# Kernel optimization log

Hardware: AMD Instinct MI355X
Metric: run time of the kernel (lower is better)

## Reference

```python
import jax, jax.numpy as jnp
import numpy as np

NUM_HEADS = 4
LN_EPS = 1e-5
L2_EPS = 1e-12


def setup_inputs() -> dict:
    key = jax.random.key(0)
    ks = jax.random.split(key, 10)
    B, L, D, Hd = 256, 197, 768, 512
    dh = Hd // NUM_HEADS  # 128
    NC = 1000
    sc = lambda k, shape, s: jax.random.normal(k, shape, jnp.float32) * s
    return {
        "cls_token": jax.random.normal(ks[0], (B, D), jnp.float32),
        "x": jax.random.normal(ks[1], (B, L, D), jnp.float32),
        "proj_w": sc(ks[2], (D, Hd), 0.02),
        "proj_b": jnp.zeros((Hd,), jnp.float32),
        "ln_g": jnp.ones((dh,), jnp.float32),
        "ln_b": jnp.zeros((dh,), jnp.float32),
        "conv1_w": sc(ks[3], (3, 3, 3, 3), 0.2),
        "conv2_w": sc(ks[4], (3, 3, 3, 3), 0.2),
        "cls1_w": sc(ks[5], (D, NC), 0.02),
        "cls1_b": jnp.zeros((NC,), jnp.float32),
        "cls2_w": sc(ks[6], (2883, NC), 0.02),
        "cls2_b": jnp.zeros((NC,), jnp.float32),
    }


def reference(cls_token, x, proj_w, proj_b, ln_g, ln_b, conv1_w, conv2_w,
              cls1_w, cls1_b, cls2_w, cls2_b):
    B, L, D = x.shape
    dh = ln_g.shape[0]
    # proj on patch tokens (drop cls at position 0)
    xp = x[:, 1:, :] @ proj_w + proj_b            # (B, 196, 512)
    Lp = xp.shape[1]
    H = xp.shape[2] // dh
    heads = xp.reshape(B, Lp, H, dh).transpose(2, 0, 1, 3)  # (H, B, Lp, dh)
    # LayerNorm over last dim (eps=1e-5, biased var, affine)
    mu = heads.mean(-1, keepdims=True)
    var = heads.var(-1, keepdims=True)
    hn = (heads - mu) * jax.lax.rsqrt(var + LN_EPS) * ln_g + ln_b
    # Covariance._remove_mean: adaptive_avg_pool2d on (B, dh, Lp) -> mean over BOTH dh and Lp per sample
    hn = hn - hn.mean(axis=(2, 3), keepdims=True)
    # 'near' cross-covariances between adjacent heads, all pairs batched
    x1, x2 = hn[:-1], hn[1:]                      # (H-1, B, Lp, dh)
    cov = jnp.einsum('pbnd,pbne->pbde', x1, x2) / Lp  # (H-1, B, dh, dh)
    # L2 normalize over dim=2 (row axis of each dh x dh map), F.normalize eps
    nrm = jnp.sqrt(jnp.sum(cov * cov, axis=2, keepdims=True))
    cov = cov / jnp.maximum(nrm, L2_EPS)
    cov = cov.transpose(1, 0, 2, 3)               # (B, 3, 128, 128)
    conv = lambda z, w: jax.lax.conv_general_dilated(
        z, w, (2, 2), 'VALID', dimension_numbers=('NCHW', 'OIHW', 'NCHW'))
    z = conv(cov, conv1_w)                        # (B, 3, 63, 63)
    z = jax.nn.gelu(z, approximate=False)
    z = conv(z, conv2_w)                          # (B, 3, 31, 31)
    flat = z.reshape(B, -1)                       # (B, 2883)
    out = ((cls_token @ cls1_w + cls1_b) + (flat @ cls2_w + cls2_b)) / 2
    return out
```

## Files before the change

kernel.cpp:

```cpp
#include <hip/hip_runtime.h>
#include <hip/hip_bf16.h>
#include <cstdint>

typedef __bf16 bf16_t;
typedef __bf16 bf16x4 __attribute__((ext_vector_type(4)));
typedef __bf16 bf16x8 __attribute__((ext_vector_type(8)));
typedef float floatx4 __attribute__((ext_vector_type(4)));

#define LNEPS 1e-5f

__device__ inline void async_copy16(const bf16_t* g, bf16_t* l) {
    __builtin_amdgcn_global_load_lds((const __attribute__((address_space(1))) void*)g,
                                     (__attribute__((address_space(3))) void*)l,
                                     16, 0, 0);
}

__global__ __launch_bounds__(256)
void k_cvt_x(const float* __restrict__ x, bf16_t* __restrict__ xbf, int b0) {
    const int vid = blockIdx.x * 256 + threadIdx.x;
    const int row = vid / 192;
    const int kv  = vid - row * 192;
    const int b = b0 + row / 196, l = row - (row / 196) * 196;
    const floatx4 f = *(const floatx4*)(x + ((b * 197 + l + 1) * 192 + kv) * 4);
    bf16x4 o;
#pragma unroll
    for (int e = 0; e < 4; e++) o[e] = (bf16_t)f[e];
    *(bf16x4*)(xbf + vid * 4) = o;
}

__global__ __launch_bounds__(256)
void k_transpose_w(const float* __restrict__ w, bf16_t* __restrict__ wt) {
    __shared__ bf16_t tile[32][33];
    const int bx = blockIdx.x;
    const int by = blockIdx.y;
    const int tx = threadIdx.x & 31, ty = threadIdx.x >> 5;
    for (int i = ty; i < 32; i += 8)
        tile[i][tx] = (bf16_t)w[(by*32 + i)*512 + bx*32 + tx];
    __syncthreads();
    for (int i = ty; i < 32; i += 8)
        wt[(bx*32 + i)*768 + by*32 + tx] = tile[tx][i];
}

__global__ __launch_bounds__(256, 2)
void k_proj_ln(const bf16_t* __restrict__ xbf, const bf16_t* __restrict__ wt,
               const float* __restrict__ pb, const float* __restrict__ lng,
               const float* __restrict__ lnb, bf16_t* __restrict__ hn, int m_base)
{
    __shared__ bf16_t As[128*32];
    __shared__ bf16_t Bs[128*32];
    __shared__ float rs_sum[2][128];
    __shared__ float rs_sq[2][128];

    const int t = threadIdx.x;
    const int lane = t & 63;
    const int wv = t >> 6;
    const int wr = wv >> 1, wc = wv & 1;
    const int q = lane >> 4;
    const int c = lane & 15;
    const int h = blockIdx.y;
    const int mt = blockIdx.x;

    const int srow  = t >> 2;
    const int skoff = (t & 3) * 8;
    const int m0 = mt * 128;
    const bf16_t* ag0 = xbf + (m0 + srow) * 768 + skoff;
    const bf16_t* ag1 = xbf + (m0 + srow + 64) * 768 + skoff;
    const bf16_t* bg0 = wt + (h*128 + srow)*768 + skoff;
    const bf16_t* bg1 = wt + (h*128 + srow + 64)*768 + skoff;

    floatx4 acc[4][4];
#pragma unroll
    for (int i = 0; i < 4; i++)
#pragma unroll
        for (int j = 0; j < 4; j++)
#pragma unroll
            for (int r = 0; r < 4; r++) acc[i][j][r] = 0.f;

    for (int k0 = 0; k0 < 768; k0 += 32) {
        __syncthreads();
        async_copy16(ag0 + k0, &As[t*8]);
        async_copy16(ag1 + k0, &As[2048 + t*8]);
        async_copy16(bg0 + k0, &Bs[t*8]);
        async_copy16(bg1 + k0, &Bs[2048 + t*8]);
        __syncthreads();
        bf16x8 af[4], bfr[4];
#pragma unroll
        for (int i = 0; i < 4; i++)
            af[i] = *(const bf16x8*)&As[(wr*64 + i*16 + c)*32 + q*8];
#pragma unroll
        for (int j = 0; j < 4; j++)
            bfr[j] = *(const bf16x8*)&Bs[(wc*64 + j*16 + c)*32 + q*8];
#pragma unroll
        for (int i = 0; i < 4; i++)
#pragma unroll
            for (int j = 0; j < 4; j++)
                acc[i][j] = __builtin_amdgcn_mfma_f32_16x16x32_bf16(af[i], bfr[j], acc[i][j], 0, 0, 0);
    }

    float bias[4], gg[4], bb[4];
#pragma unroll
    for (int j = 0; j < 4; j++) {
        const int d = wc*64 + j*16 + c;
        bias[j] = pb[h*128 + d];
        gg[j]   = lng[d];
        bb[j]   = lnb[d];
    }
#pragma unroll
    for (int i = 0; i < 4; i++)
#pragma unroll
        for (int j = 0; j < 4; j++)
#pragma unroll
            for (int r = 0; r < 4; r++) acc[i][j][r] += bias[j];

#pragma unroll
    for (int i = 0; i < 4; i++) {
#pragma unroll
        for (int r = 0; r < 4; r++) {
            float s = 0.f, s2 = 0.f;
#pragma unroll
            for (int j = 0; j < 4; j++) { const float v = acc[i][j][r]; s += v; s2 += v*v; }
#pragma unroll
            for (int o = 1; o < 16; o <<= 1) { s += __shfl_xor(s, o); s2 += __shfl_xor(s2, o); }
            if (c == 0) {
                const int row = wr*64 + i*16 + q*4 + r;
                rs_sum[wc][row] = s;
                rs_sq[wc][row]  = s2;
            }
        }
    }
    __syncthreads();
#pragma unroll
    for (int i = 0; i < 4; i++) {
#pragma unroll
        for (int r = 0; r < 4; r++) {
            const int row = wr*64 + i*16 + q*4 + r;
            const float mu = (rs_sum[0][row] + rs_sum[1][row]) * (1.f/128.f);
            const float ms = (rs_sq[0][row]  + rs_sq[1][row])  * (1.f/128.f);
            const float rstd = rsqrtf(ms - mu*mu + LNEPS);
            const int gm = m_base + m0 + row;
            const int bI = gm / 196, l = gm - bI*196;
            bf16_t* dst = hn + (((h*256 + bI)*196 + l) << 7);
#pragma unroll
            for (int j = 0; j < 4; j++) {
                const float v = (acc[i][j][r] - mu)*rstd*gg[j] + bb[j];
                dst[wc*64 + j*16 + c] = (bf16_t)v;
            }
        }
    }
}

__global__ __launch_bounds__(256, 2)
void k_cov(const bf16_t* __restrict__ hn, float* __restrict__ cov)
{
    __shared__ bf16_t x1s[128*40];
    __shared__ bf16_t x2s[128*40];
    __shared__ float rs1[128], rs2[128];
    __shared__ float colsq[2][128];
    __shared__ float nrm_inv[128];
    __shared__ float mu_s[2];

    const int t = threadIdx.x;
    const int lane = t & 63;
    const int wv = t >> 6;
    const int wr = wv >> 1, wc = wv & 1;
    const int q = lane >> 4;
    const int c = lane & 15;
    const int b = blockIdx.x;
    const int p = blockIdx.y;

    const bf16_t* X1 = hn + (((p*256 + b)*196) << 7);
    const bf16_t* X2 = hn + ((((p+1)*256 + b)*196) << 7);

    {
        const bf16_t* S = (t < 128) ? X1 : X2;
        const int d = t & 127;
        float s = 0.f;
        for (int n = 0; n < 196; n++) s += (float)S[(n << 7) + d];
        if (t < 128) rs1[d] = s; else rs2[d] = s;
    }
    __syncthreads();
    if (wv == 0) {
        float s = rs1[lane] + rs1[lane + 64];
#pragma unroll
        for (int o = 1; o < 64; o <<= 1) s += __shfl_xor(s, o);
        if (lane == 0) mu_s[0] = s * (1.f/(196.f*128.f));
    } else if (wv == 1) {
        float s = rs2[lane] + rs2[lane + 64];
#pragma unroll
        for (int o = 1; o < 64; o <<= 1) s += __shfl_xor(s, o);
        if (lane == 0) mu_s[1] = s * (1.f/(196.f*128.f));
    }

    floatx4 acc[4][4];
#pragma unroll
    for (int i = 0; i < 4; i++)
#pragma unroll
        for (int j = 0; j < 4; j++)
#pragma unroll
            for (int r = 0; r < 4; r++) acc[i][j][r] = 0.f;

    const int nl = t >> 3;
    const int d0 = (t & 7) * 16;

    for (int n0 = 0; n0 < 224; n0 += 32) {
        __syncthreads();
        const int n = n0 + nl;
        bf16x8 va, vb, wa, wb;
        if (n < 196) {
            const bf16_t* s1 = X1 + (n << 7) + d0;
            const bf16_t* s2 = X2 + (n << 7) + d0;
            va = *(const bf16x8*)s1;
            vb = *(const bf16x8*)(s1 + 8);
            wa = *(const bf16x8*)s2;
            wb = *(const bf16x8*)(s2 + 8);
        } else {
#pragma unroll
            for (int e = 0; e < 8; e++) {
                va[e] = (bf16_t)0.f; vb[e] = (bf16_t)0.f;
                wa[e] = (bf16_t)0.f; wb[e] = (bf16_t)0.f;
            }
        }
#pragma unroll
        for (int e = 0; e < 8; e++) {
            x1s[(d0 + e)*40 + nl]     = va[e];
            x1s[(d0 + 8 + e)*40 + nl] = vb[e];
            x2s[(d0 + e)*40 + nl]     = wa[e];
            x2s[(d0 + 8 + e)*40 + nl] = wb[e];
        }
        __syncthreads();
        bf16x8 af[4], bfr[4];
#pragma unroll
        for (int i = 0; i < 4; i++)
            af[i] = *(const bf16x8*)&x1s[(wr*64 + i*16 + c)*40 + q*8];
#pragma unroll
        for (int j = 0; j < 4; j++)
            bfr[j] = *(const bf16x8*)&x2s[(wc*64 + j*16 + c)*40 + q*8];
#pragma unroll
        for (int i = 0; i < 4; i++)
#pragma unroll
            for (int j = 0; j < 4; j++)
                acc[i][j] = __builtin_amdgcn_mfma_f32_16x16x32_bf16(af[i], bfr[j], acc[i][j], 0, 0, 0);
    }

    const float mu1 = mu_s[0], mu2 = mu_s[1];
    const float invL = 1.f/196.f;
    float csq[4] = {0.f, 0.f, 0.f, 0.f};
#pragma unroll
    for (int i = 0; i < 4; i++)
#pragma unroll
        for (int j = 0; j < 4; j++)
#pragma unroll
            for (int r = 0; r < 4; r++) {
                const int d = wr*64 + i*16 + q*4 + r;
                const int e = wc*64 + j*16 + c;
                const float v = acc[i][j][r]*invL - mu2*rs1[d]*invL - mu1*rs2[e]*invL + mu1*mu2;
                acc[i][j][r] = v;
                csq[j] += v*v;
            }
#pragma unroll
    for (int j = 0; j < 4; j++) {
        float s = csq[j];
        s += __shfl_xor(s, 16);
        s += __shfl_xor(s, 32);
        csq[j] = s;
    }
    if (q == 0) {
#pragma unroll
        for (int j = 0; j < 4; j++) colsq[wr][wc*64 + j*16 + c] = csq[j];
    }
    __syncthreads();
    if (t < 128) {
        const float nr = sqrtf(colsq[0][t] + colsq[1][t]);
        nrm_inv[t] = 1.f / fmaxf(nr, 1e-12f);
    }
    __syncthreads();
    float* dst = cov + ((long)b*3 + p)*16384;
#pragma unroll
    for (int i = 0; i < 4; i++)
#pragma unroll
        for (int j = 0; j < 4; j++) {
            const int e = wc*64 + j*16 + c;
            const float ni = nrm_inv[e];
#pragma unroll
            for (int r = 0; r < 4; r++) {
                const int d = wr*64 + i*16 + q*4 + r;
                dst[(d << 7) + e] = acc[i][j][r] * ni;
            }
        }
}

__global__ __launch_bounds__(256)
void k_conv1(const float* __restrict__ cov, const float* __restrict__ w1,
             float* __restrict__ z1)
{
    __shared__ float W[27];
    const int t = threadIdx.x;
    const int b = blockIdx.x, o = blockIdx.y;
    if (t < 27) W[t] = w1[o*27 + t];
    __syncthreads();
    const float* C = cov + (long)b*3*16384;
    float* Z = z1 + ((long)b*3 + o)*3969;
    for (int idx = t; idx < 3969; idx += 256) {
        const int y = idx / 63, xx = idx - y*63;
        float a = 0.f;
#pragma unroll
        for (int i = 0; i < 3; i++) {
            const float* Ci = C + i*16384 + (2*y)*128 + 2*xx;
            const float* Wi = &W[i*9];
            a += Ci[0]*Wi[0]   + Ci[1]*Wi[1]   + Ci[2]*Wi[2]
               + Ci[128]*Wi[3] + Ci[129]*Wi[4] + Ci[130]*Wi[5]
               + Ci[256]*Wi[6] + Ci[257]*Wi[7] + Ci[258]*Wi[8];
        }
        Z[idx] = 0.5f*a*(1.0f + erff(a*0.70710678118654752f));
    }
}

__global__ __launch_bounds__(256)
void k_conv2(const float* __restrict__ z1, const float* __restrict__ w2,
             bf16_t* __restrict__ Xb)
{
    __shared__ float Z[3*3969];
    __shared__ float W[81];
    const int t = threadIdx.x, b = blockIdx.x;
    if (t < 81) W[t] = w2[t];
    const float* src = z1 + (long)b*3*3969;
    for (int idx = t; idx < 3*3969; idx += 256) Z[idx] = src[idx];
    __syncthreads();
    for (int idx = t; idx < 2883; idx += 256) {
        const int o = idx / 961, rem = idx - o*961;
        const int y = rem / 31, xx = rem - y*31;
        float a = 0.f;
#pragma unroll
        for (int i = 0; i < 3; i++) {
            const float* Zi = Z + i*3969 + (2*y)*63 + 2*xx;
            const float* Wi = &W[(o*3+i)*9];
            a += Zi[0]*Wi[0]   + Zi[1]*Wi[1]   + Zi[2]*Wi[2]
               + Zi[63]*Wi[3]  + Zi[64]*Wi[4]  + Zi[65]*Wi[5]
               + Zi[126]*Wi[6] + Zi[127]*Wi[7] + Zi[128]*Wi[8];
        }
        Xb[(long)b*3712 + 768 + idx] = (bf16_t)a;
    }
}

__global__ __launch_bounds__(256)
void k_cvt_cls(const float* __restrict__ cls, bf16_t* __restrict__ Xb)
{
    const int t = threadIdx.x, b = blockIdx.x;
    for (int k = t; k < 768; k += 256)
        Xb[b*3712 + k] = (bf16_t)cls[b*768 + k];
    if (t < 61) Xb[b*3712 + 3651 + t] = (bf16_t)0.f;
}

__global__ __launch_bounds__(256)
void k_cvt_w(const float* __restrict__ W1, const float* __restrict__ W2,
             bf16_t* __restrict__ Wb)
{
    __shared__ bf16_t tile[32][33];
    const int k0 = blockIdx.x * 32;
    const int n0 = blockIdx.y * 32;
    const int tx = threadIdx.x & 31, ty = threadIdx.x >> 5;
    for (int i = ty; i < 32; i += 8) {
        const int k = k0 + i, n = n0 + tx;
        float v = 0.f;
        if (n < 1000 && k < 3651)
            v = (k < 768) ? W1[k*1000 + n] : W2[(k-768)*1000 + n];
        tile[i][tx] = (bf16_t)v;
    }
    __syncthreads();
    for (int i = ty; i < 32; i += 8)
        Wb[(n0 + i)*3712 + k0 + tx] = tile[tx][i];
}

__global__ __launch_bounds__(256, 2)
void k_gemm_cls(const bf16_t* __restrict__ Xb, const bf16_t* __restrict__ Wb,
                float* __restrict__ partial)
{
    __shared__ bf16_t As[128*32];
    __shared__ bf16_t Bs[128*32];

    const int t = threadIdx.x;
    const int lane = t & 63;
    const int wv = t >> 6;
    const int wr = wv >> 1, wc = wv & 1;
    const int q = lane >> 4;
    const int c = lane & 15;
    const int nt = blockIdx.x;
    const int mt = blockIdx.y;
    const int sp = blockIdx.z;

    const int srow  = t >> 2;
    const int skoff = (t & 3) * 8;
    const int m0 = mt * 128, n0 = nt * 128;
    const int kbase = sp * 928;
    const bf16_t* ag0 = Xb + (m0 + srow) * 3712 + kbase + skoff;
    const bf16_t* ag1 = Xb + (m0 + srow + 64) * 3712 + kbase + skoff;
    const bf16_t* bg0 = Wb + (n0 + srow) * 3712 + kbase + skoff;
    const bf16_t* bg1 = Wb + (n0 + srow + 64) * 3712 + kbase + skoff;

    floatx4 acc[4][4];
#pragma unroll
    for (int i = 0; i < 4; i++)
#pragma unroll
        for (int j = 0; j < 4; j++)
#pragma unroll
            for (int r = 0; r < 4; r++) acc[i][j][r] = 0.f;

    for (int k0 = 0; k0 < 928; k0 += 32) {
        __syncthreads();
        async_copy16(ag0 + k0, &As[t*8]);
        async_copy16(ag1 + k0, &As[2048 + t*8]);
        async_copy16(bg0 + k0, &Bs[t*8]);
        async_copy16(bg1 + k0, &Bs[2048 + t*8]);
        __syncthreads();
        bf16x8 af[4], bfr[4];
#pragma unroll
        for (int i = 0; i < 4; i++)
            af[i] = *(const bf16x8*)&As[(wr*64 + i*16 + c)*32 + q*8];
#pragma unroll
        for (int j = 0; j < 4; j++)
            bfr[j] = *(const bf16x8*)&Bs[(wc*64 + j*16 + c)*32 + q*8];
#pragma unroll
        for (int i = 0; i < 4; i++)
#pragma unroll
            for (int j = 0; j < 4; j++)
                acc[i][j] = __builtin_amdgcn_mfma_f32_16x16x32_bf16(af[i], bfr[j], acc[i][j], 0, 0, 0);
    }

    float* base = partial + ((long)sp*256 + m0)*1024 + n0;
#pragma unroll
    for (int i = 0; i < 4; i++)
#pragma unroll
        for (int r = 0; r < 4; r++) {
            const int row = wr*64 + i*16 + q*4 + r;
#pragma unroll
            for (int j = 0; j < 4; j++)
                base[row*1024 + wc*64 + j*16 + c] = acc[i][j][r];
        }
}

__global__ __launch_bounds__(256)
void k_cls_fin(const float* __restrict__ partial, const float* __restrict__ b1,
               const float* __restrict__ b2, float* __restrict__ out)
{
    const int idx = blockIdx.x * 256 + threadIdx.x;
    const int m = idx / 1000, n = idx - m*1000;
    float s = partial[(m)*1024 + n] + partial[(256 + m)*1024 + n]
            + partial[(512 + m)*1024 + n] + partial[(768 + m)*1024 + n];
    out[idx] = 0.5f*(s + b1[n] + b2[n]);
}

extern "C" void kernel_launch(void* const* d_in, const int* in_sizes, int n_in,
                              void* d_out, int out_size, void* d_ws, size_t ws_size,
                              hipStream_t stream) {
    const float* cls = (const float*)d_in[0];
    const float* x   = (const float*)d_in[1];
    const float* pw  = (const float*)d_in[2];
    const float* pb  = (const float*)d_in[3];
    const float* lng = (const float*)d_in[4];
    const float* lnb = (const float*)d_in[5];
    const float* c1w = (const float*)d_in[6];
    const float* c2w = (const float*)d_in[7];
    const float* w1  = (const float*)d_in[8];
    const float* b1  = (const float*)d_in[9];
    const float* w2  = (const float*)d_in[10];
    const float* b2  = (const float*)d_in[11];

    char* ws = (char*)d_ws;
    bf16_t* hn    = (bf16_t*)(ws);
    bf16_t* xbfh  = (bf16_t*)(ws + 51380224ull);
    bf16_t* wt    = (bf16_t*)(ws + 89915392ull);
    float*  covb  = (float*) (ws + 51380224ull);
    float*  z1    = (float*) (ws);
    bf16_t* Xb    = (bf16_t*)(ws + 101711872ull);
    bf16_t* Wb    = (bf16_t*)(ws + 103612416ull);
    float*  part  = (float*) (ws + 111214592ull);
    float*  out   = (float*)d_out;

    k_transpose_w<<<dim3(16, 24), 256, 0, stream>>>(pw, wt);
    k_cvt_x<<<18816, 256, 0, stream>>>(x, xbfh, 0);
    k_proj_ln<<<dim3(196, 4), 256, 0, stream>>>(xbfh, wt, pb, lng, lnb, hn, 0);
    k_cvt_x<<<18816, 256, 0, stream>>>(x, xbfh, 128);
    k_proj_ln<<<dim3(196, 4), 256, 0, stream>>>(xbfh, wt, pb, lng, lnb, hn, 25088);
    k_cvt_cls<<<256, 256, 0, stream>>>(cls, Xb);
    k_cvt_w<<<dim3(116, 32), 256, 0, stream>>>(w1, w2, Wb);
    k_cov<<<dim3(256, 3), 256, 0, stream>>>(hn, covb);
    k_conv1<<<dim3(256, 3), 256, 0, stream>>>(covb, c1w, z1);
    k_conv2<<<256, 256, 0, stream>>>(z1, c2w, Xb);
    k_gemm_cls<<<dim3(8, 2, 4), 256, 0, stream>>>(Xb, Wb, part);
    k_cls_fin<<<1000, 256, 0, stream>>>(part, b1, b2, out);
}
```

Measured before the change: 441.1 us.

## Widen proj tile to two heads, fuse convs, precompute column sums

The x conversion now runs once over the whole batch with 8-wide vectors instead of two half-batch passes, and the projection GEMM runs as a single launch. Each projection block now covers two full heads (256 columns), so each wave owns one head and can do the LayerNorm reduction with shuffles alone, dropping the shared-memory row-stat pass and its barrier. A separate column-sum kernel precomputes per-sample sums so the covariance kernel no longer does a serial 196-row scan twice per block. conv1 and conv2 are fused so the GELU output stays in shared memory instead of going through global memory. The cost is a doubled accumulator array per thread (more VGPR pressure at 2 blocks/SM) and a larger workspace footprint.

```diff
diff --git a/kernel.cpp b/kernel.cpp
--- a/kernel.cpp
+++ b/kernel.cpp
@@ -16,16 +16,18 @@
 }
 
 __global__ __launch_bounds__(256)
-void k_cvt_x(const float* __restrict__ x, bf16_t* __restrict__ xbf, int b0) {
+void k_cvt_x(const float* __restrict__ x, bf16_t* __restrict__ xbf) {
     const int vid = blockIdx.x * 256 + threadIdx.x;
-    const int row = vid / 192;
-    const int kv  = vid - row * 192;
-    const int b = b0 + row / 196, l = row - (row / 196) * 196;
-    const floatx4 f = *(const floatx4*)(x + ((b * 197 + l + 1) * 192 + kv) * 4);
-    bf16x4 o;
-#pragma unroll
-    for (int e = 0; e < 4; e++) o[e] = (bf16_t)f[e];
-    *(bf16x4*)(xbf + vid * 4) = o;
+    const int row = vid / 96;
+    const int kv  = vid - row * 96;
+    const int b = row / 196, l = row - (row / 196) * 196;
+    const float* src = x + ((b * 197 + l + 1) * 96 + kv) * 8;
+    const floatx4 f0 = *(const floatx4*)src;
+    const floatx4 f1 = *(const floatx4*)(src + 4);
+    bf16x8 o;
+#pragma unroll
+    for (int e = 0; e < 4; e++) { o[e] = (bf16_t)f0[e]; o[e+4] = (bf16_t)f1[e]; }
+    *(bf16x8*)(xbf + vid * 8) = o;
 }
 
 __global__ __launch_bounds__(256)
@@ -44,12 +46,10 @@
 __global__ __launch_bounds__(256, 2)
 void k_proj_ln(const bf16_t* __restrict__ xbf, const bf16_t* __restrict__ wt,
                const float* __restrict__ pb, const float* __restrict__ lng,
-               const float* __restrict__ lnb, bf16_t* __restrict__ hn, int m_base)
+               const float* __restrict__ lnb, bf16_t* __restrict__ hn)
 {
     __shared__ bf16_t As[128*32];
-    __shared__ bf16_t Bs[128*32];
-    __shared__ float rs_sum[2][128];
-    __shared__ float rs_sq[2][128];
+    __shared__ bf16_t Bs[256*32];
 
     const int t = threadIdx.x;
     const int lane = t & 63;
@@ -57,22 +57,20 @@
     const int wr = wv >> 1, wc = wv & 1;
     const int q = lane >> 4;
     const int c = lane & 15;
-    const int h = blockIdx.y;
-    const int mt = blockIdx.x;
+    const int hp = blockIdx.y;
+    const int m0 = blockIdx.x * 128;
 
     const int srow  = t >> 2;
     const int skoff = (t & 3) * 8;
-    const int m0 = mt * 128;
     const bf16_t* ag0 = xbf + (m0 + srow) * 768 + skoff;
-    const bf16_t* ag1 = xbf + (m0 + srow + 64) * 768 + skoff;
-    const bf16_t* bg0 = wt + (h*128 + srow)*768 + skoff;
-    const bf16_t* bg1 = wt + (h*128 + srow + 64)*768 + skoff;
-
-    floatx4 acc[4][4];
-#pragma unroll
-    for (int i = 0; i < 4; i++)
-#pragma unroll
-        for (int j = 0; j < 4; j++)
+    const bf16_t* ag1 = ag0 + 64*768;
+    const bf16_t* bg0 = wt + (hp*256 + srow)*768 + skoff;
+
+    floatx4 acc[4][8];
+#pragma unroll
+    for (int i = 0; i < 4; i++)
+#pragma unroll
+        for (int j = 0; j < 8; j++)
 #pragma unroll
             for (int r = 0; r < 4; r++) acc[i][j][r] = 0.f;
 
@@ -80,77 +78,80 @@
         __syncthreads();
         async_copy16(ag0 + k0, &As[t*8]);
         async_copy16(ag1 + k0, &As[2048 + t*8]);
-        async_copy16(bg0 + k0, &Bs[t*8]);
-        async_copy16(bg1 + k0, &Bs[2048 + t*8]);
-        __syncthreads();
-        bf16x8 af[4], bfr[4];
+        async_copy16(bg0 + k0,            &Bs[t*8]);
+        async_copy16(bg0 + 64*768 + k0,   &Bs[2048 + t*8]);
+        async_copy16(bg0 + 128*768 + k0,  &Bs[4096 + t*8]);
+        async_copy16(bg0 + 192*768 + k0,  &Bs[6144 + t*8]);
+        __syncthreads();
+        bf16x8 af[4], bfr[8];
 #pragma unroll
         for (int i = 0; i < 4; i++)
             af[i] = *(const bf16x8*)&As[(wr*64 + i*16 + c)*32 + q*8];
 #pragma unroll
-        for (int j = 0; j < 4; j++)
-            bfr[j] = *(const bf16x8*)&Bs[(wc*64 + j*16 + c)*32 + q*8];
-#pragma unroll
-        for (int i = 0; i < 4; i++)
-#pragma unroll
-            for (int j = 0; j < 4; j++)
+        for (int j = 0; j < 8; j++)
+            bfr[j] = *(const bf16x8*)&Bs[(wc*128 + j*16 + c)*32 + q*8];
+#pragma unroll
+        for (int i = 0; i < 4; i++)
+#pragma unroll
+            for (int j = 0; j < 8; j++)
                 acc[i][j] = __builtin_amdgcn_mfma_f32_16x16x32_bf16(af[i], bfr[j], acc[i][j], 0, 0, 0);
     }
 
-    float bias[4], gg[4], bb[4];
-#pragma unroll
-    for (int j = 0; j < 4; j++) {
-        const int d = wc*64 + j*16 + c;
+    const int h = hp*2 + wc;
+    float bias[8], gg[8], bb[8];
+#pragma unroll
+    for (int j = 0; j < 8; j++) {
+        const int d = j*16 + c;
         bias[j] = pb[h*128 + d];
         gg[j]   = lng[d];
         bb[j]   = lnb[d];
     }
 #pragma unroll
-    for (int i = 0; i < 4; i++)
-#pragma unroll
-        for (int j = 0; j < 4; j++)
-#pragma unroll
-            for (int r = 0; r < 4; r++) acc[i][j][r] += bias[j];
-
-#pragma unroll
     for (int i = 0; i < 4; i++) {
 #pragma unroll
         for (int r = 0; r < 4; r++) {
             float s = 0.f, s2 = 0.f;
 #pragma unroll
-            for (int j = 0; j < 4; j++) { const float v = acc[i][j][r]; s += v; s2 += v*v; }
+            for (int j = 0; j < 8; j++) {
+                const float v = acc[i][j][r] + bias[j];
+                acc[i][j][r] = v;
+                s += v; s2 += v*v;
+            }
 #pragma unroll
             for (int o = 1; o < 16; o <<= 1) { s += __shfl_xor(s, o); s2 += __shfl_xor(s2, o); }
-            if (c == 0) {
-                const int row = wr*64 + i*16 + q*4 + r;
-                rs_sum[wc][row] = s;
-                rs_sq[wc][row]  = s2;
-            }
-        }
-    }
-    __syncthreads();
-#pragma unroll
-    for (int i = 0; i < 4; i++) {
-#pragma unroll
-        for (int r = 0; r < 4; r++) {
-            const int row = wr*64 + i*16 + q*4 + r;
-            const float mu = (rs_sum[0][row] + rs_sum[1][row]) * (1.f/128.f);
-            const float ms = (rs_sq[0][row]  + rs_sq[1][row])  * (1.f/128.f);
+            const float mu = s * (1.f/128.f);
+            const float ms = s2 * (1.f/128.f);
             const float rstd = rsqrtf(ms - mu*mu + LNEPS);
-            const int gm = m_base + m0 + row;
+            const int gm = m0 + wr*64 + i*16 + q*4 + r;
             const int bI = gm / 196, l = gm - bI*196;
             bf16_t* dst = hn + (((h*256 + bI)*196 + l) << 7);
 #pragma unroll
-            for (int j = 0; j < 4; j++) {
+            for (int j = 0; j < 8; j++) {
                 const float v = (acc[i][j][r] - mu)*rstd*gg[j] + bb[j];
-                dst[wc*64 + j*16 + c] = (bf16_t)v;
+                dst[j*16 + c] = (bf16_t)v;
             }
         }
     }
 }
 
+__global__ __launch_bounds__(256)
+void k_colsum(const bf16_t* __restrict__ hn, float* __restrict__ colsum)
+{
+    __shared__ float tmp[2][128];
+    const int t = threadIdx.x;
+    const int d = t & 127, half = t >> 7;
+    const bf16_t* S = hn + ((long)blockIdx.x * 196 << 7);
+    float s = 0.f;
+    const int n0 = half * 98;
+    for (int n = 0; n < 98; n++) s += (float)S[((n0 + n) << 7) + d];
+    tmp[half][d] = s;
+    __syncthreads();
+    if (t < 128) colsum[(blockIdx.x << 7) + t] = tmp[0][t] + tmp[1][t];
+}
+
 __global__ __launch_bounds__(256, 2)
-void k_cov(const bf16_t* __restrict__ hn, float* __restrict__ cov)
+void k_cov(const bf16_t* __restrict__ hn, const float* __restrict__ colsum,
+           float* __restrict__ cov)
 {
     __shared__ bf16_t x1s[128*40];
     __shared__ bf16_t x2s[128*40];
@@ -171,13 +172,8 @@
     const bf16_t* X1 = hn + (((p*256 + b)*196) << 7);
     const bf16_t* X2 = hn + ((((p+1)*256 + b)*196) << 7);
 
-    {
-        const bf16_t* S = (t < 128) ? X1 : X2;
-        const int d = t & 127;
-        float s = 0.f;
-        for (int n = 0; n < 196; n++) s += (float)S[(n << 7) + d];
-        if (t < 128) rs1[d] = s; else rs2[d] = s;
-    }
+    if (t < 128) rs1[t] = colsum[((p*256 + b) << 7) + t];
+    else         rs2[t & 127] = colsum[(((p+1)*256 + b) << 7) + (t & 127)];
     __syncthreads();
     if (wv == 0) {
         float s = rs1[lane] + rs1[lane + 64];
@@ -290,41 +286,30 @@
 }
 
 __global__ __launch_bounds__(256)
-void k_conv1(const float* __restrict__ cov, const float* __restrict__ w1,
-             float* __restrict__ z1)
-{
-    __shared__ float W[27];
-    const int t = threadIdx.x;
-    const int b = blockIdx.x, o = blockIdx.y;
-    if (t < 27) W[t] = w1[o*27 + t];
+void k_convs(const float* __restrict__ cov, const float* __restrict__ w1,
+             const float* __restrict__ w2, bf16_t* __restrict__ Xb)
+{
+    __shared__ float Z[3*3969];
+    __shared__ float W1s[81];
+    __shared__ float W2s[81];
+    const int t = threadIdx.x, b = blockIdx.x;
+    if (t < 81) { W1s[t] = w1[t]; W2s[t] = w2[t]; }
     __syncthreads();
     const float* C = cov + (long)b*3*16384;
-    float* Z = z1 + ((long)b*3 + o)*3969;
-    for (int idx = t; idx < 3969; idx += 256) {
-        const int y = idx / 63, xx = idx - y*63;
+    for (int idx = t; idx < 3*3969; idx += 256) {
+        const int o = idx / 3969, rem = idx - o*3969;
+        const int y = rem / 63, xx = rem - y*63;
         float a = 0.f;
 #pragma unroll
         for (int i = 0; i < 3; i++) {
             const float* Ci = C + i*16384 + (2*y)*128 + 2*xx;
-            const float* Wi = &W[i*9];
+            const float* Wi = &W1s[o*27 + i*9];
             a += Ci[0]*Wi[0]   + Ci[1]*Wi[1]   + Ci[2]*Wi[2]
                + Ci[128]*Wi[3] + Ci[129]*Wi[4] + Ci[130]*Wi[5]
                + Ci[256]*Wi[6] + Ci[257]*Wi[7] + Ci[258]*Wi[8];
         }
         Z[idx] = 0.5f*a*(1.0f + erff(a*0.70710678118654752f));
     }
-}
-
-__global__ __launch_bounds__(256)
-void k_conv2(const float* __restrict__ z1, const float* __restrict__ w2,
-             bf16_t* __restrict__ Xb)
-{
-    __shared__ float Z[3*3969];
-    __shared__ float W[81];
-    const int t = threadIdx.x, b = blockIdx.x;
-    if (t < 81) W[t] = w2[t];
-    const float* src = z1 + (long)b*3*3969;
-    for (int idx = t; idx < 3*3969; idx += 256) Z[idx] = src[idx];
     __syncthreads();
     for (int idx = t; idx < 2883; idx += 256) {
         const int o = idx / 961, rem = idx - o*961;
@@ -333,7 +318,7 @@
 #pragma unroll
         for (int i = 0; i < 3; i++) {
             const float* Zi = Z + i*3969 + (2*y)*63 + 2*xx;
-            const float* Wi = &W[(o*3+i)*9];
+            const float* Wi = &W2s[(o*3+i)*9];
             a += Zi[0]*Wi[0]   + Zi[1]*Wi[1]   + Zi[2]*Wi[2]
                + Zi[63]*Wi[3]  + Zi[64]*Wi[4]  + Zi[65]*Wi[5]
                + Zi[126]*Wi[6] + Zi[127]*Wi[7] + Zi[128]*Wi[8];
@@ -467,25 +452,23 @@
 
     char* ws = (char*)d_ws;
     bf16_t* hn    = (bf16_t*)(ws);
-    bf16_t* xbfh  = (bf16_t*)(ws + 51380224ull);
-    bf16_t* wt    = (bf16_t*)(ws + 89915392ull);
+    bf16_t* xbf   = (bf16_t*)(ws + 51380224ull);
+    bf16_t* wt    = (bf16_t*)(ws + 128450560ull);
     float*  covb  = (float*) (ws + 51380224ull);
-    float*  z1    = (float*) (ws);
-    bf16_t* Xb    = (bf16_t*)(ws + 101711872ull);
-    bf16_t* Wb    = (bf16_t*)(ws + 103612416ull);
-    float*  part  = (float*) (ws + 111214592ull);
+    float*  csum  = (float*) (ws + 129236992ull);
+    bf16_t* Xb    = (bf16_t*)(ws + 129761280ull);
+    bf16_t* Wb    = (bf16_t*)(ws + 131661824ull);
+    float*  part  = (float*) (ws + 139264000ull);
     float*  out   = (float*)d_out;
 
     k_transpose_w<<<dim3(16, 24), 256, 0, stream>>>(pw, wt);
-    k_cvt_x<<<18816, 256, 0, stream>>>(x, xbfh, 0);
-    k_proj_ln<<<dim3(196, 4), 256, 0, stream>>>(xbfh, wt, pb, lng, lnb, hn, 0);
-    k_cvt_x<<<18816, 256, 0, stream>>>(x, xbfh, 128);
-    k_proj_ln<<<dim3(196, 4), 256, 0, stream>>>(xbfh, wt, pb, lng, lnb, hn, 25088);
+    k_cvt_x<<<18816, 256, 0, stream>>>(x, xbf);
     k_cvt_cls<<<256, 256, 0, stream>>>(cls, Xb);
     k_cvt_w<<<dim3(116, 32), 256, 0, stream>>>(w1, w2, Wb);
-    k_cov<<<dim3(256, 3), 256, 0, stream>>>(hn, covb);
-    k_conv1<<<dim3(256, 3), 256, 0, stream>>>(covb, c1w, z1);
-    k_conv2<<<256, 256, 0, stream>>>(z1, c2w, Xb);
+    k_proj_ln<<<dim3(392, 2), 256, 0, stream>>>(xbf, wt, pb, lng, lnb, hn);
+    k_colsum<<<1024, 256, 0, stream>>>(hn, csum);
+    k_cov<<<dim3(256, 3), 256, 0, stream>>>(hn, csum, covb);
+    k_convs<<<256, 256, 0, stream>>>(covb, c1w, c2w, Xb);
     k_gemm_cls<<<dim3(8, 2, 4), 256, 0, stream>>>(Xb, Wb, part);
     k_cls_fin<<<1000, 256, 0, stream>>>(part, b1, b2, out);
 }
```

Result: no change. 433.2 us (-1.8%).
